# Optimization experiments

Hardware: AMD Instinct MI355X
Metric: run time of the kernel (lower is better)

## Reference

```python
import jax, jax.numpy as jnp
import numpy as np

D_MODEL = 1024
N_HEADS = 16
HEAD_DIM = D_MODEL // N_HEADS
FF_DIM = 1024  # repo bug: linear2 is Linear(d_model, ff_dim); ff_dim==d_model required for residual
EPS = 1e-5


def _linear_params(k, d_in, d_out):
    kw, kb = jax.random.split(k)
    bound = 1.0 / np.sqrt(d_in)
    W = jax.random.uniform(kw, (d_out, d_in), minval=-bound, maxval=bound, dtype=jnp.float32)
    b = jax.random.uniform(kb, (d_out,), minval=-bound, maxval=bound, dtype=jnp.float32)
    return W, b


def setup_inputs() -> dict:
    key = jax.random.key(0)
    ks = jax.random.split(key, 8)
    src = jax.random.normal(ks[0], (4, 2048, D_MODEL), dtype=jnp.float32)
    Wq, bq = _linear_params(ks[1], D_MODEL, D_MODEL)
    Wk, bk = _linear_params(ks[2], D_MODEL, D_MODEL)
    Wv, bv = _linear_params(ks[3], D_MODEL, D_MODEL)
    Wo, bo = _linear_params(ks[4], D_MODEL, D_MODEL)
    W1, b1 = _linear_params(ks[5], D_MODEL, FF_DIM)
    W2, b2 = _linear_params(ks[6], D_MODEL, FF_DIM)
    g1 = jnp.ones((D_MODEL,), jnp.float32); be1 = jnp.zeros((D_MODEL,), jnp.float32)
    g2 = jnp.ones((D_MODEL,), jnp.float32); be2 = jnp.zeros((D_MODEL,), jnp.float32)
    return {"src": src, "Wq": Wq, "bq": bq, "Wk": Wk, "bk": bk, "Wv": Wv, "bv": bv,
            "Wo": Wo, "bo": bo, "W1": W1, "b1": b1, "W2": W2, "b2": b2,
            "g1": g1, "be1": be1, "g2": g2, "be2": be2}


def _layernorm(x, g, b):
    mu = jnp.mean(x, axis=-1, keepdims=True)
    var = jnp.var(x, axis=-1, keepdims=True)
    return (x - mu) * jax.lax.rsqrt(var + EPS) * g + b


def _mha(x, Wq, bq, Wk, bk, Wv, bv, Wo, bo):
    B, S, _ = x.shape
    def proj(W, b):
        return (x @ W.T + b).reshape(B, S, N_HEADS, HEAD_DIM).transpose(0, 2, 1, 3)
    Q, K, V = proj(Wq, bq), proj(Wk, bk), proj(Wv, bv)
    scale = jnp.float32(np.sqrt(HEAD_DIM))
    energy = jnp.einsum('bhqd,bhkd->bhqk', Q, K) / scale
    attn = jax.nn.softmax(energy, axis=-1)
    out = jnp.einsum('bhqk,bhkd->bhqd', attn, V)
    out = out.transpose(0, 2, 1, 3).reshape(B, S, D_MODEL)
    return out @ Wo.T + bo


def reference(src, Wq, bq, Wk, bk, Wv, bv, Wo, bo, W1, b1, W2, b2, g1, be1, g2, be2):
    x = src
    x = x + _mha(_layernorm(x, g1, be1), Wq, bq, Wk, bk, Wv, bv, Wo, bo)
    h = _layernorm(x, g2, be2)
    ff = jax.nn.relu(h @ W1.T + b1) @ W2.T + b2
    return x + ff
```

## Files before the change

### kernel.cpp

```cpp
#include <hip/hip_runtime.h>
#include <stdint.h>

typedef __attribute__((ext_vector_type(8))) short    bf16x8;
typedef __attribute__((ext_vector_type(4))) short    bf16x4;
typedef __attribute__((ext_vector_type(4))) float    f32x4;
typedef __attribute__((ext_vector_type(8))) uint16_t u16x8;
typedef __attribute__((ext_vector_type(4))) uint16_t u16x4;

#define D_MODEL 1024
#define SEQ     2048
#define NB      4
#define NH      16
#define HD      64
#define MTOK    8192

__device__ __forceinline__ float bf2f(uint16_t u) {
    union { uint32_t i; float f; } x; x.i = ((uint32_t)u) << 16; return x.f;
}
__device__ __forceinline__ uint16_t f2bf(float f) {
    union { float f; uint32_t i; } x; x.f = f;
    uint32_t r = (x.i + 0x7fffu + ((x.i >> 16) & 1u)) >> 16;
    return (uint16_t)r;
}
__device__ __forceinline__ void gload16(const void* g, void* l) {
    __builtin_amdgcn_global_load_lds(
        (const __attribute__((address_space(1))) unsigned int*)g,
        (__attribute__((address_space(3))) unsigned int*)l, 16, 0, 0);
}
__device__ __forceinline__ bf16x8 lds_ld8(const uint16_t* p) {
    bf16x4 a = *(const bf16x4*)p;
    bf16x4 b = *(const bf16x4*)(p + 4);
    bf16x8 r;
    r[0] = a[0]; r[1] = a[1]; r[2] = a[2]; r[3] = a[3];
    r[4] = b[0]; r[5] = b[1]; r[6] = b[2]; r[7] = b[3];
    return r;
}

__global__ __launch_bounds__(256)
void cvt_w(const float* __restrict__ in, uint16_t* __restrict__ out)
{
    const int i = (blockIdx.x * 256 + threadIdx.x) * 4;
    float4 v = *(const float4*)(in + i);
    u16x4 o;
    o[0] = f2bf(v.x); o[1] = f2bf(v.y); o[2] = f2bf(v.z); o[3] = f2bf(v.w);
    *(u16x4*)(out + i) = o;
}

__global__ __launch_bounds__(256)
void ln_kernel(const float* __restrict__ x, const float* __restrict__ g,
               const float* __restrict__ be, uint16_t* __restrict__ y)
{
    const int row = blockIdx.x;
    const int tid = threadIdx.x;
    const size_t base = (size_t)row * D_MODEL + tid * 4;
    float4 v = *(const float4*)(x + base);
    float f[4] = {v.x, v.y, v.z, v.w};
    float sum = 0.f, sq = 0.f;
#pragma unroll
    for (int e = 0; e < 4; e++) { sum += f[e]; sq += f[e] * f[e]; }
#pragma unroll
    for (int o = 32; o > 0; o >>= 1) { sum += __shfl_down(sum, o); sq += __shfl_down(sq, o); }
    __shared__ float ps[4], pq[4];
    const int lane = tid & 63, wid = tid >> 6;
    if (lane == 0) { ps[wid] = sum; pq[wid] = sq; }
    __syncthreads();
    const float ts = ps[0] + ps[1] + ps[2] + ps[3];
    const float tq = pq[0] + pq[1] + pq[2] + pq[3];
    const float mean = ts * (1.0f / D_MODEL);
    const float var  = tq * (1.0f / D_MODEL) - mean * mean;
    const float rstd = rsqrtf(var + 1e-5f);
    float4 gv = *(const float4*)(g + tid * 4);
    float4 bv = *(const float4*)(be + tid * 4);
    const float gg[4] = {gv.x, gv.y, gv.z, gv.w};
    const float bb[4] = {bv.x, bv.y, bv.z, bv.w};
    u16x4 outv;
#pragma unroll
    for (int e = 0; e < 4; e++)
        outv[e] = f2bf((f[e] - mean) * rstd * gg[e] + bb[e]);
    *(u16x4*)(y + base) = outv;
}

template<int RESID, int RELU, int OUTF32>
__global__ __launch_bounds__(256, 2)
void gemm_bt(const uint16_t* __restrict__ A, const uint16_t* __restrict__ W,
             const float* __restrict__ bias, const float* __restrict__ resid,
             void* __restrict__ Cv, float alpha)
{
    __shared__ uint16_t lA[128 * 32];
    __shared__ uint16_t lB[128 * 32];
    const int tid  = threadIdx.x;
    const int lane = tid & 63;
    const int quad = lane >> 4;
    const int l16  = lane & 15;
    const int wid  = tid >> 6;
    const int wm   = wid >> 1;
    const int wn   = wid & 1;
    const int m0   = blockIdx.y * 128;
    const int n0   = blockIdx.x * 128;

    f32x4 acc[4][4];
#pragma unroll
    for (int i = 0; i < 4; i++)
#pragma unroll
        for (int j = 0; j < 4; j++) acc[i][j] = (f32x4){0.f, 0.f, 0.f, 0.f};

    const int sr = tid >> 2;
    const int sc = (tid & 3) * 8;
    const uint16_t* gA0 = A + (size_t)(m0 + sr) * D_MODEL + sc;
    const uint16_t* gA1 = gA0 + (size_t)64 * D_MODEL;
    const uint16_t* gW0 = W + (size_t)(n0 + sr) * D_MODEL + sc;
    const uint16_t* gW1 = gW0 + (size_t)64 * D_MODEL;
    uint16_t* sA0 = &lA[tid * 8];
    uint16_t* sA1 = sA0 + 2048;
    uint16_t* sB0 = &lB[tid * 8];
    uint16_t* sB1 = sB0 + 2048;

    for (int k0 = 0; k0 < D_MODEL; k0 += 32) {
        __syncthreads();
        gload16(gA0 + k0, sA0);
        gload16(gA1 + k0, sA1);
        gload16(gW0 + k0, sB0);
        gload16(gW1 + k0, sB1);
        __syncthreads();
        bf16x8 af[4], bfr[4];
#pragma unroll
        for (int i = 0; i < 4; i++)
            af[i] = *(const bf16x8*)&lA[(wm * 64 + i * 16 + l16) * 32 + quad * 8];
#pragma unroll
        for (int j = 0; j < 4; j++)
            bfr[j] = *(const bf16x8*)&lB[(wn * 64 + j * 16 + l16) * 32 + quad * 8];
#pragma unroll
        for (int i = 0; i < 4; i++)
#pragma unroll
            for (int j = 0; j < 4; j++)
                acc[i][j] = __builtin_amdgcn_mfma_f32_16x16x32_bf16(af[i], bfr[j], acc[i][j], 0, 0, 0);
    }

#pragma unroll
    for (int j = 0; j < 4; j++) {
        const int col = n0 + wn * 64 + j * 16 + l16;
        const float bv = bias[col];
#pragma unroll
        for (int i = 0; i < 4; i++) {
            const int row = m0 + wm * 64 + i * 16 + quad * 4;
#pragma unroll
            for (int r = 0; r < 4; r++) {
                float v = (acc[i][j][r] + bv) * alpha;
                const size_t idx = (size_t)(row + r) * D_MODEL + col;
                if (RESID) v += resid[idx];
                if (RELU)  v = fmaxf(v, 0.0f);
                if (OUTF32) ((float*)Cv)[idx] = v;
                else        ((uint16_t*)Cv)[idx] = f2bf(v);
            }
        }
    }
}

__global__ __launch_bounds__(256, 2)
void gemm_vt(const uint16_t* __restrict__ A, const uint16_t* __restrict__ W,
             const float* __restrict__ bias, uint16_t* __restrict__ Vt)
{
    __shared__ uint16_t lW[128 * 32];
    __shared__ uint16_t lX[128 * 32];
    const int tid  = threadIdx.x;
    const int lane = tid & 63;
    const int quad = lane >> 4;
    const int l16  = lane & 15;
    const int wid  = tid >> 6;
    const int wm   = wid >> 1;
    const int wn   = wid & 1;
    const int t0   = blockIdx.x * 128;
    const int w0   = blockIdx.y * 128;

    f32x4 acc[4][4];
#pragma unroll
    for (int i = 0; i < 4; i++)
#pragma unroll
        for (int j = 0; j < 4; j++) acc[i][j] = (f32x4){0.f, 0.f, 0.f, 0.f};

    const int sr = tid >> 2;
    const int sc = (tid & 3) * 8;
    const uint16_t* gW0 = W + (size_t)(w0 + sr) * D_MODEL + sc;
    const uint16_t* gW1 = gW0 + (size_t)64 * D_MODEL;
    const uint16_t* gX0 = A + (size_t)(t0 + sr) * D_MODEL + sc;
    const uint16_t* gX1 = gX0 + (size_t)64 * D_MODEL;
    uint16_t* sW0 = &lW[tid * 8];
    uint16_t* sW1 = sW0 + 2048;
    uint16_t* sX0 = &lX[tid * 8];
    uint16_t* sX1 = sX0 + 2048;

    for (int k0 = 0; k0 < D_MODEL; k0 += 32) {
        __syncthreads();
        gload16(gW0 + k0, sW0);
        gload16(gW1 + k0, sW1);
        gload16(gX0 + k0, sX0);
        gload16(gX1 + k0, sX1);
        __syncthreads();
        bf16x8 wf[4], xf[4];
#pragma unroll
        for (int i = 0; i < 4; i++)
            wf[i] = *(const bf16x8*)&lW[(wm * 64 + i * 16 + l16) * 32 + quad * 8];
#pragma unroll
        for (int j = 0; j < 4; j++)
            xf[j] = *(const bf16x8*)&lX[(wn * 64 + j * 16 + l16) * 32 + quad * 8];
#pragma unroll
        for (int i = 0; i < 4; i++)
#pragma unroll
            for (int j = 0; j < 4; j++)
                acc[i][j] = __builtin_amdgcn_mfma_f32_16x16x32_bf16(wf[i], xf[j], acc[i][j], 0, 0, 0);
    }

#pragma unroll
    for (int i = 0; i < 4; i++) {
#pragma unroll
        for (int r = 0; r < 4; r++) {
            const int wrow = w0 + wm * 64 + i * 16 + quad * 4 + r;
            const float bv = bias[wrow];
#pragma unroll
            for (int j = 0; j < 4; j++) {
                const int tok = t0 + wn * 64 + j * 16 + l16;
                Vt[(size_t)wrow * MTOK + tok] = f2bf(acc[i][j][r] + bv);
            }
        }
    }
}

#define PST 68
__global__ __launch_bounds__(256, 4)
void attn_kernel(const uint16_t* __restrict__ Q, const uint16_t* __restrict__ K,
                 const uint16_t* __restrict__ Vt, uint16_t* __restrict__ O)
{
    __shared__ uint16_t sQP[128 * PST];
    __shared__ uint16_t sK [64 * PST];
    __shared__ uint16_t sVt[64 * PST];
    __shared__ float    sSt[128];

    const int tid  = threadIdx.x;
    const int lane = tid & 63;
    const int quad = lane >> 4;
    const int l16  = lane & 15;
    const int w    = tid >> 6;

    const int q0 = blockIdx.x * 128;
    const int h  = blockIdx.y;
    const int b  = blockIdx.z;
    const size_t headoff = (size_t)h * HD;
    const size_t bbase   = (size_t)b * SEQ;

    const int r8 = tid >> 3;
    const int c8 = (tid & 7) * 8;

#pragma unroll
    for (int i = 0; i < 4; i++)
        gload16(Q + (bbase + q0 + i * 32 + r8) * D_MODEL + headoff + c8, &sQP[i * 2048 + tid * 8]);
    __syncthreads();

    bf16x8 qa[2][2];
#pragma unroll
    for (int i = 0; i < 2; i++)
#pragma unroll
        for (int ks = 0; ks < 2; ks++)
            qa[i][ks] = *(const bf16x8*)&sQP[(w * 32 + i * 16 + l16) * 64 + ks * 32 + quad * 8];

    f32x4 oacc[2][4];
#pragma unroll
    for (int i = 0; i < 2; i++)
#pragma unroll
        for (int n = 0; n < 4; n++) oacc[i][n] = (f32x4){0.f, 0.f, 0.f, 0.f};
    float mrun[2] = {-3.0e38f, -3.0e38f};
    float lrun[2] = {0.f, 0.f};

    const uint16_t* gK  = K  + bbase * D_MODEL + headoff;
    const uint16_t* gVt = Vt + headoff * MTOK + bbase;

    for (int kv0 = 0; kv0 < SEQ; kv0 += 64) {
        u16x8 kreg[2], vreg[2];
#pragma unroll
        for (int i = 0; i < 2; i++) {
            const int row = i * 32 + r8;
            kreg[i] = *(const u16x8*)(gK + (size_t)(kv0 + row) * D_MODEL + c8);
            vreg[i] = *(const u16x8*)(gVt + (size_t)row * MTOK + kv0 + c8);
        }
        __syncthreads();
#pragma unroll
        for (int i = 0; i < 2; i++) {
            const int row = i * 32 + r8;
            *(u16x4*)&sK [(size_t)row * PST + c8]     = (u16x4){kreg[i][0], kreg[i][1], kreg[i][2], kreg[i][3]};
            *(u16x4*)&sK [(size_t)row * PST + c8 + 4] = (u16x4){kreg[i][4], kreg[i][5], kreg[i][6], kreg[i][7]};
            *(u16x4*)&sVt[(size_t)row * PST + c8]     = (u16x4){vreg[i][0], vreg[i][1], vreg[i][2], vreg[i][3]};
            *(u16x4*)&sVt[(size_t)row * PST + c8 + 4] = (u16x4){vreg[i][4], vreg[i][5], vreg[i][6], vreg[i][7]};
        }
        __syncthreads();

        f32x4 st[4][2];
#pragma unroll
        for (int j = 0; j < 4; j++)
#pragma unroll
            for (int i = 0; i < 2; i++) st[j][i] = (f32x4){0.f, 0.f, 0.f, 0.f};
#pragma unroll
        for (int ks = 0; ks < 2; ks++)
#pragma unroll
            for (int j = 0; j < 4; j++) {
                bf16x8 kb = lds_ld8(&sK[(j * 16 + l16) * PST + ks * 32 + quad * 8]);
#pragma unroll
                for (int i = 0; i < 2; i++)
                    st[j][i] = __builtin_amdgcn_mfma_f32_16x16x32_bf16(kb, qa[i][ks], st[j][i], 0, 0, 0);
            }

#pragma unroll
        for (int i = 0; i < 2; i++) {
            float mx = -3.0e38f;
#pragma unroll
            for (int j = 0; j < 4; j++)
#pragma unroll
                for (int r = 0; r < 4; r++) mx = fmaxf(mx, st[j][i][r]);
            mx = fmaxf(mx, __shfl_xor(mx, 16));
            mx = fmaxf(mx, __shfl_xor(mx, 32));
            const float mnew = fmaxf(mrun[i], mx);
            const float al   = __expf(mrun[i] - mnew);
            float rs = 0.f;
#pragma unroll
            for (int j = 0; j < 4; j++)
#pragma unroll
                for (int r = 0; r < 4; r++) {
                    const float p = __expf(st[j][i][r] - mnew);
                    st[j][i][r] = p;
                    rs += p;
                }
            rs += __shfl_xor(rs, 16);
            rs += __shfl_xor(rs, 32);
            lrun[i] = lrun[i] * al + rs;
            mrun[i] = mnew;
            sSt[w * 32 + i * 16 + l16] = al;
#pragma unroll
            for (int j = 0; j < 4; j++) {
                u16x4 pv;
#pragma unroll
                for (int r = 0; r < 4; r++) pv[r] = f2bf(st[j][i][r]);
                *(u16x4*)&sQP[(size_t)(w * 32 + i * 16 + l16) * PST + j * 16 + quad * 4] = pv;
            }
        }

#pragma unroll
        for (int i = 0; i < 2; i++)
#pragma unroll
            for (int r = 0; r < 4; r++) {
                const float al = sSt[w * 32 + i * 16 + quad * 4 + r];
#pragma unroll
                for (int n = 0; n < 4; n++) oacc[i][n][r] *= al;
            }

#pragma unroll
        for (int i = 0; i < 2; i++)
#pragma unroll
            for (int ks = 0; ks < 2; ks++) {
                bf16x8 pa = lds_ld8(&sQP[(size_t)(w * 32 + i * 16 + l16) * PST + ks * 32 + quad * 8]);
#pragma unroll
                for (int n = 0; n < 4; n++) {
                    bf16x8 vb = lds_ld8(&sVt[(n * 16 + l16) * PST + ks * 32 + quad * 8]);
                    oacc[i][n] = __builtin_amdgcn_mfma_f32_16x16x32_bf16(pa, vb, oacc[i][n], 0, 0, 0);
                }
            }
    }

#pragma unroll
    for (int i = 0; i < 2; i++)
        sSt[w * 32 + i * 16 + l16] = 1.0f / lrun[i];
#pragma unroll
    for (int i = 0; i < 2; i++)
#pragma unroll
        for (int r = 0; r < 4; r++) {
            const size_t row = bbase + q0 + w * 32 + i * 16 + quad * 4 + r;
            const float inv = sSt[w * 32 + i * 16 + quad * 4 + r];
#pragma unroll
            for (int n = 0; n < 4; n++)
                O[row * D_MODEL + headoff + n * 16 + l16] = f2bf(oacc[i][n][r] * inv);
        }
}

extern "C" void kernel_launch(void* const* d_in, const int* in_sizes, int n_in,
                              void* d_out, int out_size, void* d_ws, size_t ws_size,
                              hipStream_t stream)
{
    const float* src = (const float*)d_in[0];
    const float* Wq  = (const float*)d_in[1];
    const float* bq  = (const float*)d_in[2];
    const float* Wk  = (const float*)d_in[3];
    const float* bk  = (const float*)d_in[4];
    const float* Wv  = (const float*)d_in[5];
    const float* bv  = (const float*)d_in[6];
    const float* Wo  = (const float*)d_in[7];
    const float* bo  = (const float*)d_in[8];
    const float* W1  = (const float*)d_in[9];
    const float* b1  = (const float*)d_in[10];
    const float* W2  = (const float*)d_in[11];
    const float* b2  = (const float*)d_in[12];
    const float* g1  = (const float*)d_in[13];
    const float* be1 = (const float*)d_in[14];
    const float* g2  = (const float*)d_in[15];
    const float* be2 = (const float*)d_in[16];
    float* out = (float*)d_out;

    uint16_t* ws  = (uint16_t*)d_ws;
    const size_t BUF = (size_t)MTOK * D_MODEL;
    const size_t WSZ = (size_t)D_MODEL * D_MODEL;
    uint16_t* xn1 = ws;
    uint16_t* Vtb = ws + BUF;
    uint16_t* wWq = ws + 2 * BUF;
    uint16_t* wWk = wWq + WSZ;
    uint16_t* wWv = wWk + WSZ;
    uint16_t* wWo = wWv + WSZ;
    uint16_t* wW1 = wWo + WSZ;
    uint16_t* wW2 = wW1 + WSZ;
    uint16_t* Qb  = (uint16_t*)d_out;
    uint16_t* Kb  = Qb + BUF;
    float*    x2  = (float*)d_out;

    dim3 gblk(8, 64), blk(256);
    cvt_w<<<1024, 256, 0, stream>>>(Wq, wWq);
    cvt_w<<<1024, 256, 0, stream>>>(Wk, wWk);
    cvt_w<<<1024, 256, 0, stream>>>(Wv, wWv);
    cvt_w<<<1024, 256, 0, stream>>>(Wo, wWo);
    cvt_w<<<1024, 256, 0, stream>>>(W1, wW1);
    cvt_w<<<1024, 256, 0, stream>>>(W2, wW2);

    ln_kernel<<<8192, 256, 0, stream>>>(src, g1, be1, xn1);
    gemm_bt<0, 0, 0><<<gblk, blk, 0, stream>>>(xn1, wWq, bq, nullptr, Qb, 0.125f);
    gemm_bt<0, 0, 0><<<gblk, blk, 0, stream>>>(xn1, wWk, bk, nullptr, Kb, 1.0f);
    gemm_vt<<<dim3(64, 8), blk, 0, stream>>>(xn1, wWv, bv, Vtb);
    attn_kernel<<<dim3(16, NH, NB), 256, 0, stream>>>(Qb, Kb, Vtb, xn1);
    gemm_bt<1, 0, 1><<<gblk, blk, 0, stream>>>(xn1, wWo, bo, src, x2, 1.0f);
    ln_kernel<<<8192, 256, 0, stream>>>(x2, g2, be2, xn1);
    gemm_bt<0, 1, 0><<<gblk, blk, 0, stream>>>(xn1, wW1, b1, nullptr, Vtb, 1.0f);
    gemm_bt<1, 0, 1><<<gblk, blk, 0, stream>>>(Vtb, wW2, b2, x2, out, 1.0f);
}
```

Measured before the change: 447.6 us.

## Fuse QKV projections into one GEMM launch, batch weight casts, use exp2 softmax

Merges the six weight-conversion launches into one 2D-grid kernel, and the Q, K and transposed-V projections into a single GEMM over a concatenated weight buffer. The grid grows to 24x64 blocks and each block picks its operand order and output layout by column range. The Q scale now folds in log2(e), so softmax can use exp2f, and probabilities are packed to bf16 by truncation through a byte permute. This cuts launch count and tail effects and makes the softmax inner loop cheaper. In exchange it adds a branch per k-step in the GEMM and slightly less accurate bf16 rounding of the probabilities.

After: 431.5 us. 1.04x faster.

```diff
diff --git a/kernel.cpp b/kernel.cpp
--- a/kernel.cpp
+++ b/kernel.cpp
@@ -35,10 +35,22 @@
     r[4] = b[0]; r[5] = b[1]; r[6] = b[2]; r[7] = b[3];
     return r;
 }
+__device__ __forceinline__ uint32_t pk_bf16_trunc(float lo, float hi) {
+    return __builtin_amdgcn_perm(__float_as_uint(hi), __float_as_uint(lo), 0x07060302u);
+}
 
 __global__ __launch_bounds__(256)
-void cvt_w(const float* __restrict__ in, uint16_t* __restrict__ out)
-{
+void cvt_all(const float* __restrict__ s0, const float* __restrict__ s1,
+             const float* __restrict__ s2, const float* __restrict__ s3,
+             const float* __restrict__ s4, const float* __restrict__ s5,
+             uint16_t* __restrict__ dQKV, uint16_t* __restrict__ dWo,
+             uint16_t* __restrict__ dW1, uint16_t* __restrict__ dW2)
+{
+    const float* srcs[6] = {s0, s1, s2, s3, s4, s5};
+    uint16_t* dsts[6] = {dQKV, dQKV + (size_t)D_MODEL * D_MODEL,
+                         dQKV + 2 * (size_t)D_MODEL * D_MODEL, dWo, dW1, dW2};
+    const float* in = srcs[blockIdx.y];
+    uint16_t* out = dsts[blockIdx.y];
     const int i = (blockIdx.x * 256 + threadIdx.x) * 4;
     float4 v = *(const float4*)(in + i);
     u16x4 o;
@@ -156,12 +168,15 @@
     }
 }
 
-__global__ __launch_bounds__(256, 2)
-void gemm_vt(const uint16_t* __restrict__ A, const uint16_t* __restrict__ W,
-             const float* __restrict__ bias, uint16_t* __restrict__ Vt)
-{
-    __shared__ uint16_t lW[128 * 32];
-    __shared__ uint16_t lX[128 * 32];
+#define QSCALE 0.18033688f
+__global__ __launch_bounds__(256, 3)
+void gemm_qkv(const uint16_t* __restrict__ A, const uint16_t* __restrict__ Wqkv,
+              const float* __restrict__ bq, const float* __restrict__ bk,
+              const float* __restrict__ bv, uint16_t* __restrict__ Qb,
+              uint16_t* __restrict__ Kb, uint16_t* __restrict__ Vt)
+{
+    __shared__ uint16_t lA[128 * 32];
+    __shared__ uint16_t lB[128 * 32];
     const int tid  = threadIdx.x;
     const int lane = tid & 63;
     const int quad = lane >> 4;
@@ -169,8 +184,10 @@
     const int wid  = tid >> 6;
     const int wm   = wid >> 1;
     const int wn   = wid & 1;
-    const int t0   = blockIdx.x * 128;
-    const int w0   = blockIdx.y * 128;
+    const int t0   = blockIdx.y * 128;
+    const int n0   = blockIdx.x * 128;
+    const int which = n0 >> 10;
+    const int lc0   = n0 & 1023;
 
     f32x4 acc[4][4];
 #pragma unroll
@@ -180,46 +197,73 @@
 
     const int sr = tid >> 2;
     const int sc = (tid & 3) * 8;
-    const uint16_t* gW0 = W + (size_t)(w0 + sr) * D_MODEL + sc;
+    const uint16_t* gA0 = A + (size_t)(t0 + sr) * D_MODEL + sc;
+    const uint16_t* gA1 = gA0 + (size_t)64 * D_MODEL;
+    const uint16_t* gW0 = Wqkv + (size_t)(n0 + sr) * D_MODEL + sc;
     const uint16_t* gW1 = gW0 + (size_t)64 * D_MODEL;
-    const uint16_t* gX0 = A + (size_t)(t0 + sr) * D_MODEL + sc;
-    const uint16_t* gX1 = gX0 + (size_t)64 * D_MODEL;
-    uint16_t* sW0 = &lW[tid * 8];
-    uint16_t* sW1 = sW0 + 2048;
-    uint16_t* sX0 = &lX[tid * 8];
-    uint16_t* sX1 = sX0 + 2048;
+    uint16_t* sA0 = &lA[tid * 8];
+    uint16_t* sA1 = sA0 + 2048;
+    uint16_t* sB0 = &lB[tid * 8];
+    uint16_t* sB1 = sB0 + 2048;
 
     for (int k0 = 0; k0 < D_MODEL; k0 += 32) {
         __syncthreads();
-        gload16(gW0 + k0, sW0);
-        gload16(gW1 + k0, sW1);
-        gload16(gX0 + k0, sX0);
-        gload16(gX1 + k0, sX1);
-        __syncthreads();
-        bf16x8 wf[4], xf[4];
+        gload16(gA0 + k0, sA0);
+        gload16(gA1 + k0, sA1);
+        gload16(gW0 + k0, sB0);
+        gload16(gW1 + k0, sB1);
+        __syncthreads();
+        bf16x8 fa[4], fb[4];
+        if (which != 2) {
+#pragma unroll
+            for (int i = 0; i < 4; i++)
+                fa[i] = *(const bf16x8*)&lA[(wm * 64 + i * 16 + l16) * 32 + quad * 8];
+#pragma unroll
+            for (int j = 0; j < 4; j++)
+                fb[j] = *(const bf16x8*)&lB[(wn * 64 + j * 16 + l16) * 32 + quad * 8];
+        } else {
+#pragma unroll
+            for (int i = 0; i < 4; i++)
+                fa[i] = *(const bf16x8*)&lB[(wm * 64 + i * 16 + l16) * 32 + quad * 8];
+#pragma unroll
+            for (int j = 0; j < 4; j++)
+                fb[j] = *(const bf16x8*)&lA[(wn * 64 + j * 16 + l16) * 32 + quad * 8];
+        }
 #pragma unroll
         for (int i = 0; i < 4; i++)
-            wf[i] = *(const bf16x8*)&lW[(wm * 64 + i * 16 + l16) * 32 + quad * 8];
-#pragma unroll
-        for (int j = 0; j < 4; j++)
-            xf[j] = *(const bf16x8*)&lX[(wn * 64 + j * 16 + l16) * 32 + quad * 8];
-#pragma unroll
-        for (int i = 0; i < 4; i++)
-#pragma unroll
-            for (int j = 0; j < 4; j++)
-                acc[i][j] = __builtin_amdgcn_mfma_f32_16x16x32_bf16(wf[i], xf[j], acc[i][j], 0, 0, 0);
+#pragma unroll
+            for (int j = 0; j < 4; j++)
+                acc[i][j] = __builtin_amdgcn_mfma_f32_16x16x32_bf16(fa[i], fb[j], acc[i][j], 0, 0, 0);
     }
 
-#pragma unroll
-    for (int i = 0; i < 4; i++) {
-#pragma unroll
-        for (int r = 0; r < 4; r++) {
-            const int wrow = w0 + wm * 64 + i * 16 + quad * 4 + r;
-            const float bv = bias[wrow];
-#pragma unroll
-            for (int j = 0; j < 4; j++) {
-                const int tok = t0 + wn * 64 + j * 16 + l16;
-                Vt[(size_t)wrow * MTOK + tok] = f2bf(acc[i][j][r] + bv);
+    if (which != 2) {
+        const float* bias = (which == 0) ? bq : bk;
+        uint16_t* C = (which == 0) ? Qb : Kb;
+        const float alpha = (which == 0) ? QSCALE : 1.0f;
+#pragma unroll
+        for (int j = 0; j < 4; j++) {
+            const int col = lc0 + wn * 64 + j * 16 + l16;
+            const float bvv = bias[col];
+#pragma unroll
+            for (int i = 0; i < 4; i++) {
+                const int row = t0 + wm * 64 + i * 16 + quad * 4;
+#pragma unroll
+                for (int r = 0; r < 4; r++)
+                    C[(size_t)(row + r) * D_MODEL + col] = f2bf((acc[i][j][r] + bvv) * alpha);
+            }
+        }
+    } else {
+#pragma unroll
+        for (int i = 0; i < 4; i++) {
+#pragma unroll
+            for (int r = 0; r < 4; r++) {
+                const int wrow = lc0 + wm * 64 + i * 16 + quad * 4 + r;
+                const float bvv = bv[wrow];
+#pragma unroll
+                for (int j = 0; j < 4; j++) {
+                    const int tok = t0 + wn * 64 + j * 16 + l16;
+                    Vt[(size_t)wrow * MTOK + tok] = f2bf(acc[i][j][r] + bvv);
+                }
             }
         }
     }
@@ -317,13 +361,13 @@
             mx = fmaxf(mx, __shfl_xor(mx, 16));
             mx = fmaxf(mx, __shfl_xor(mx, 32));
             const float mnew = fmaxf(mrun[i], mx);
-            const float al   = __expf(mrun[i] - mnew);
+            const float al   = exp2f(mrun[i] - mnew);
             float rs = 0.f;
 #pragma unroll
             for (int j = 0; j < 4; j++)
 #pragma unroll
                 for (int r = 0; r < 4; r++) {
-                    const float p = __expf(st[j][i][r] - mnew);
+                    const float p = exp2f(st[j][i][r] - mnew);
                     st[j][i][r] = p;
                     rs += p;
                 }
@@ -334,10 +378,10 @@
             sSt[w * 32 + i * 16 + l16] = al;
 #pragma unroll
             for (int j = 0; j < 4; j++) {
-                u16x4 pv;
-#pragma unroll
-                for (int r = 0; r < 4; r++) pv[r] = f2bf(st[j][i][r]);
-                *(u16x4*)&sQP[(size_t)(w * 32 + i * 16 + l16) * PST + j * 16 + quad * 4] = pv;
+                uint2 pk;
+                pk.x = pk_bf16_trunc(st[j][i][0], st[j][i][1]);
+                pk.y = pk_bf16_trunc(st[j][i][2], st[j][i][3]);
+                *(uint2*)&sQP[(size_t)(w * 32 + i * 16 + l16) * PST + j * 16 + quad * 4] = pk;
             }
         }
 
@@ -404,30 +448,20 @@
     uint16_t* ws  = (uint16_t*)d_ws;
     const size_t BUF = (size_t)MTOK * D_MODEL;
     const size_t WSZ = (size_t)D_MODEL * D_MODEL;
-    uint16_t* xn1 = ws;
-    uint16_t* Vtb = ws + BUF;
-    uint16_t* wWq = ws + 2 * BUF;
-    uint16_t* wWk = wWq + WSZ;
-    uint16_t* wWv = wWk + WSZ;
-    uint16_t* wWo = wWv + WSZ;
-    uint16_t* wW1 = wWo + WSZ;
-    uint16_t* wW2 = wW1 + WSZ;
-    uint16_t* Qb  = (uint16_t*)d_out;
-    uint16_t* Kb  = Qb + BUF;
-    float*    x2  = (float*)d_out;
+    uint16_t* xn1  = ws;
+    uint16_t* Vtb  = ws + BUF;
+    uint16_t* wQKV = ws + 2 * BUF;
+    uint16_t* wWo  = wQKV + 3 * WSZ;
+    uint16_t* wW1  = wWo + WSZ;
+    uint16_t* wW2  = wW1 + WSZ;
+    uint16_t* Qb   = (uint16_t*)d_out;
+    uint16_t* Kb   = Qb + BUF;
+    float*    x2   = (float*)d_out;
 
     dim3 gblk(8, 64), blk(256);
-    cvt_w<<<1024, 256, 0, stream>>>(Wq, wWq);
-    cvt_w<<<1024, 256, 0, stream>>>(Wk, wWk);
-    cvt_w<<<1024, 256, 0, stream>>>(Wv, wWv);
-    cvt_w<<<1024, 256, 0, stream>>>(Wo, wWo);
-    cvt_w<<<1024, 256, 0, stream>>>(W1, wW1);
-    cvt_w<<<1024, 256, 0, stream>>>(W2, wW2);
-
+    cvt_all<<<dim3(1024, 6), 256, 0, stream>>>(Wq, Wk, Wv, Wo, W1, W2, wQKV, wWo, wW1, wW2);
     ln_kernel<<<8192, 256, 0, stream>>>(src, g1, be1, xn1);
-    gemm_bt<0, 0, 0><<<gblk, blk, 0, stream>>>(xn1, wWq, bq, nullptr, Qb, 0.125f);
-    gemm_bt<0, 0, 0><<<gblk, blk, 0, stream>>>(xn1, wWk, bk, nullptr, Kb, 1.0f);
-    gemm_vt<<<dim3(64, 8), blk, 0, stream>>>(xn1, wWv, bv, Vtb);
+    gemm_qkv<<<dim3(24, 64), blk, 0, stream>>>(xn1, wQKV, bq, bk, bv, Qb, Kb, Vtb);
     attn_kernel<<<dim3(16, NH, NB), 256, 0, stream>>>(Qb, Kb, Vtb, xn1);
     gemm_bt<1, 0, 1><<<gblk, blk, 0, stream>>>(xn1, wWo, bo, src, x2, 1.0f);
     ln_kernel<<<8192, 256, 0, stream>>>(x2, g2, be2, xn1);
```
